# Kernel tuning notes

Measured on AMD Instinct MI355X. Metric: run time of the kernel, lower is better.

The kernel has to match this reference:

```python
import jax, jax.numpy as jnp
import numpy as np

B = 65536      # batch of (state, action) pairs
DIM_S = 64     # input feature dim
DIM_C = 8      # number of options / experts
H = 256        # hidden width (two hidden layers)


def setup_inputs() -> dict:
    key = jax.random.key(0)
    ks = jax.random.split(key, 7)
    s = 0.05  # small init scale
    st = jax.random.normal(ks[0], (B, DIM_S), dtype=jnp.float32)
    # Batched expert weights: one slice per expert (dim_c experts).
    W1 = jax.random.normal(ks[1], (DIM_C, DIM_S, H), dtype=jnp.float32) * s
    b1 = jax.random.normal(ks[2], (DIM_C, H), dtype=jnp.float32) * s
    W2 = jax.random.normal(ks[3], (DIM_C, H, H), dtype=jnp.float32) * s
    b2 = jax.random.normal(ks[4], (DIM_C, H), dtype=jnp.float32) * s
    W3 = jax.random.normal(ks[5], (DIM_C, H, 1), dtype=jnp.float32) * s
    b3 = jax.random.normal(ks[6], (DIM_C, 1), dtype=jnp.float32) * s
    return {"st": st, "W1": W1, "b1": b1, "W2": W2, "b2": b2,
            "W3": W3, "b3": b3}


def reference(st, W1, b1, W2, b2, W3, b3):
    # Equivalent of torch.stack([m(st) for m in self.discriminator], dim=1):
    # every expert MLP (dim_s -> H -> H -> 1, ReLU) applied to the same st,
    # expressed as batched GEMMs over the expert axis c.
    h = jax.nn.relu(jnp.einsum('bs,csh->bch', st, W1) + b1[None])   # [B, C, H]
    h = jax.nn.relu(jnp.einsum('bch,chk->bck', h, W2) + b2[None])   # [B, C, H]
    d = jnp.einsum('bch,cho->bco', h, W3) + b3[None]                # [B, C, 1]
    return d
```

## Files before the change

### kernel.cpp

```cpp
#include <hip/hip_runtime.h>
#include <hip/hip_bf16.h>

typedef __bf16 bf16x8 __attribute__((ext_vector_type(8)));
typedef float  f32x4  __attribute__((ext_vector_type(4)));

static constexpr int S  = 64;
static constexpr int C  = 8;
static constexpr int HD = 256;

__device__ __forceinline__ unsigned short f2bf(float f) {
  __hip_bfloat16 b = __float2bfloat16(f);
  unsigned short u;
  __builtin_memcpy(&u, &b, 2);
  return u;
}

__device__ __forceinline__ void gl2lds16(const void* g, void* l) {
  __builtin_amdgcn_global_load_lds(
      (const __attribute__((address_space(1))) unsigned int*)g,
      (__attribute__((address_space(3))) unsigned int*)l, 16, 0, 0);
}

__global__ __launch_bounds__(256) void prep_weights(
    const float* __restrict__ W1, const float* __restrict__ W2,
    unsigned short* __restrict__ W1T, unsigned short* __restrict__ W2T)
{
  __shared__ float tile[32][33];
  const int tid = threadIdx.x, cl = tid & 31, r0 = tid >> 5;
  const int b = blockIdx.x;
  if (b < 512) {
    const int c = b >> 6, t = b & 63, kt = t >> 3, nt = t & 7;
    const float* src = W2 + c * 65536;
    #pragma unroll
    for (int i = 0; i < 4; ++i) {
      int r = r0 + 8 * i;
      tile[r][cl] = src[(kt * 32 + r) * 256 + nt * 32 + cl];
    }
    __syncthreads();
    unsigned short* dst = W2T + c * 65536;
    #pragma unroll
    for (int i = 0; i < 4; ++i) {
      int r = r0 + 8 * i;
      dst[(nt * 32 + r) * 256 + kt * 32 + cl] = f2bf(tile[cl][r]);
    }
  } else {
    const int bb = b - 512;
    const int c = bb >> 4, t = bb & 15, st2 = t >> 3, ht = t & 7;
    const float* src = W1 + c * 16384;
    #pragma unroll
    for (int i = 0; i < 4; ++i) {
      int r = r0 + 8 * i;
      tile[r][cl] = src[(st2 * 32 + r) * 256 + ht * 32 + cl];
    }
    __syncthreads();
    unsigned short* dst = W1T + c * 16384;
    #pragma unroll
    for (int i = 0; i < 4; ++i) {
      int r = r0 + 8 * i;
      dst[(ht * 32 + r) * 64 + st2 * 32 + cl] = f2bf(tile[cl][r]);
    }
  }
}

__global__ __launch_bounds__(256, 2) void moe_fused(
    const float* __restrict__ st,
    const unsigned short* __restrict__ W1T,
    const unsigned short* __restrict__ W2T,
    const float* __restrict__ b1,
    const float* __restrict__ b2,
    const float* __restrict__ W3,
    const float* __restrict__ b3,
    float* __restrict__ out)
{
  constexpr int LDT = 72;

  __shared__ __align__(16) unsigned short sT[256 * LDT];
  __shared__ __align__(16) unsigned short sU[2 * 32 * 256];

  const int tid  = threadIdx.x;
  const int lane = tid & 63;
  const int wv   = tid >> 6;
  const int l15  = lane & 15;
  const int q    = lane >> 4;
  const int c    = blockIdx.x >> 8;
  const int row0 = (blockIdx.x & 255) * 256;

  const unsigned short* W1c = W1T + c * HD * S;
  const unsigned short* W2c = W2T + c * HD * HD;

  {
    #pragma unroll
    for (int it = 0; it < 8; ++it) {
      const int r = wv * 64 + it * 8 + (lane >> 3);
      const int g = lane & 7;
      const float4* p = reinterpret_cast<const float4*>(
          st + (size_t)(row0 + r) * S + g * 8);
      float4 x = p[0], y = p[1];
      union { uint4 u4; unsigned short us[8]; } pk;
      pk.us[0] = f2bf(x.x); pk.us[1] = f2bf(x.y); pk.us[2] = f2bf(x.z); pk.us[3] = f2bf(x.w);
      pk.us[4] = f2bf(y.x); pk.us[5] = f2bf(y.y); pk.us[6] = f2bf(y.z); pk.us[7] = f2bf(y.w);
      *reinterpret_cast<uint4*>(sU + r * 64 + ((g ^ (r & 7)) << 3)) = pk.u4;
    }
  }
  __asm__ __volatile__("s_waitcnt lgkmcnt(0)" ::: "memory");

  bf16x8 aF[4][4][2];
  #pragma unroll
  for (int cc = 0; cc < 4; ++cc) {
    f32x4 bias[4];
    #pragma unroll
    for (int mt = 0; mt < 4; ++mt)
      bias[mt] = *reinterpret_cast<const f32x4*>(
          b1 + c * HD + cc * 64 + mt * 16 + q * 4);

    f32x4 acc[4][4];
    #pragma unroll
    for (int mt = 0; mt < 4; ++mt)
      #pragma unroll
      for (int nt = 0; nt < 4; ++nt)
        acc[mt][nt] = (f32x4){0.f, 0.f, 0.f, 0.f};

    #pragma unroll
    for (int ks = 0; ks < 2; ++ks) {
      bf16x8 aW[4];
      #pragma unroll
      for (int mt = 0; mt < 4; ++mt)
        aW[mt] = *reinterpret_cast<const bf16x8*>(
            W1c + (cc * 64 + mt * 16 + l15) * S + ks * 32 + q * 8);
      bf16x8 bB[4];
      #pragma unroll
      for (int nt = 0; nt < 4; ++nt) {
        const int r = wv * 64 + nt * 16 + l15;
        const int g = ks * 4 + q;
        bB[nt] = *reinterpret_cast<const bf16x8*>(
            sU + r * 64 + ((g ^ (r & 7)) << 3));
      }
      #pragma unroll
      for (int mt = 0; mt < 4; ++mt)
        #pragma unroll
        for (int nt = 0; nt < 4; ++nt)
          acc[mt][nt] = __builtin_amdgcn_mfma_f32_16x16x32_bf16(
              aW[mt], bB[nt], acc[mt][nt], 0, 0, 0);
    }

    #pragma unroll
    for (int mt = 0; mt < 4; ++mt) {
      #pragma unroll
      for (int nt = 0; nt < 4; ++nt) {
        ushort4 pk;
        float v0 = acc[mt][nt][0] + bias[mt][0]; v0 = v0 > 0.f ? v0 : 0.f;
        float v1 = acc[mt][nt][1] + bias[mt][1]; v1 = v1 > 0.f ? v1 : 0.f;
        float v2 = acc[mt][nt][2] + bias[mt][2]; v2 = v2 > 0.f ? v2 : 0.f;
        float v3 = acc[mt][nt][3] + bias[mt][3]; v3 = v3 > 0.f ? v3 : 0.f;
        pk.x = f2bf(v0); pk.y = f2bf(v1); pk.z = f2bf(v2); pk.w = f2bf(v3);
        *reinterpret_cast<ushort4*>(
            sT + (wv * 64 + nt * 16 + l15) * LDT + mt * 16 + q * 4) = pk;
      }
    }
    __asm__ __volatile__("s_waitcnt lgkmcnt(0)" ::: "memory");
    #pragma unroll
    for (int rt = 0; rt < 4; ++rt)
      #pragma unroll
      for (int k2 = 0; k2 < 2; ++k2)
        aF[cc][rt][k2] = *reinterpret_cast<const bf16x8*>(
            sT + (wv * 64 + rt * 16 + l15) * LDT + k2 * 32 + q * 8);
    __asm__ __volatile__("s_waitcnt lgkmcnt(0)" ::: "memory");
  }

  float pb2v[8][2], pw3v[8][2];
  #pragma unroll
  for (int ch = 0; ch < 8; ++ch)
    #pragma unroll
    for (int ct = 0; ct < 2; ++ct) {
      const int n = ch * 32 + ct * 16 + l15;
      pb2v[ch][ct] = b2[c * HD + n];
      pw3v[ch][ct] = W3[c * HD + n];
    }
  const float bb3 = b3[c];

  __syncthreads();

  #pragma unroll
  for (int pc = 0; pc < 2; ++pc) {
    unsigned short* buf = sU + pc * (32 * 256);
    #pragma unroll
    for (int i = 0; i < 4; ++i) {
      const int b2i = wv * 4 + i;
      const int r   = b2i * 2 + (lane >> 5);
      const int j   = (lane & 31) ^ (r & 7);
      gl2lds16(W2c + (pc * 32 + r) * 256 + j * 8, buf + b2i * 512);
    }
  }
  __syncthreads();

  float dacc[4][4];
  #pragma unroll
  for (int rt = 0; rt < 4; ++rt)
    #pragma unroll
    for (int r = 0; r < 4; ++r) dacc[rt][r] = 0.f;

  #pragma unroll
  for (int ch = 0; ch < 8; ++ch) {
    const unsigned short* buf = sU + (ch & 1) * (32 * 256);

    f32x4 acc[4][2];
    #pragma unroll
    for (int rt = 0; rt < 4; ++rt)
      #pragma unroll
      for (int ct = 0; ct < 2; ++ct)
        acc[rt][ct] = (f32x4){0.f, 0.f, 0.f, 0.f};

    #pragma unroll
    for (int ks = 0; ks < 8; ++ks) {
      const int jj = ks * 4 + q;
      const int cc = ks >> 1, k2 = ks & 1;
      #pragma unroll
      for (int ct = 0; ct < 2; ++ct) {
        const int nl = ct * 16 + l15;
        bf16x8 b = *reinterpret_cast<const bf16x8*>(
            buf + nl * 256 + ((jj ^ (l15 & 7)) << 3));
        #pragma unroll
        for (int rt = 0; rt < 4; ++rt)
          acc[rt][ct] = __builtin_amdgcn_mfma_f32_16x16x32_bf16(
              aF[cc][rt][k2], b, acc[rt][ct], 0, 0, 0);
      }
    }

    #pragma unroll
    for (int ct = 0; ct < 2; ++ct) {
      const float bias = pb2v[ch][ct];
      const float w3v  = pw3v[ch][ct];
      #pragma unroll
      for (int rt = 0; rt < 4; ++rt)
        #pragma unroll
        for (int r = 0; r < 4; ++r) {
          float v = acc[rt][ct][r] + bias;
          v = v > 0.f ? v : 0.f;
          dacc[rt][r] += v * w3v;
        }
    }

    __syncthreads();
    if (ch < 6) {
      unsigned short* nbuf = sU + (ch & 1) * (32 * 256);
      #pragma unroll
      for (int i = 0; i < 4; ++i) {
        const int b2i = wv * 4 + i;
        const int r   = b2i * 2 + (lane >> 5);
        const int j   = (lane & 31) ^ (r & 7);
        gl2lds16(W2c + ((ch + 2) * 32 + r) * 256 + j * 8, nbuf + b2i * 512);
      }
    }
  }

  #pragma unroll
  for (int rt = 0; rt < 4; ++rt)
    #pragma unroll
    for (int r = 0; r < 4; ++r) {
      float v = dacc[rt][r];
      v += __shfl_xor(v, 1);
      v += __shfl_xor(v, 2);
      v += __shfl_xor(v, 4);
      v += __shfl_xor(v, 8);
      dacc[rt][r] = v;
    }

  if (l15 == 0) {
    const int rbase = row0 + wv * 64 + q * 4;
    #pragma unroll
    for (int rt = 0; rt < 4; ++rt)
      #pragma unroll
      for (int r = 0; r < 4; ++r)
        out[(rbase + rt * 16 + r) * C + c] = dacc[rt][r] + bb3;
  }
}

extern "C" void kernel_launch(void* const* d_in, const int* in_sizes, int n_in,
                              void* d_out, int out_size, void* d_ws, size_t ws_size,
                              hipStream_t stream)
{
  const float* st = (const float*)d_in[0];
  const float* W1 = (const float*)d_in[1];
  const float* b1 = (const float*)d_in[2];
  const float* W2 = (const float*)d_in[3];
  const float* b2 = (const float*)d_in[4];
  const float* W3 = (const float*)d_in[5];
  const float* b3 = (const float*)d_in[6];
  float* out = (float*)d_out;

  unsigned short* W1T = (unsigned short*)d_ws;
  unsigned short* W2T = W1T + C * HD * S;

  prep_weights<<<dim3(640), dim3(256), 0, stream>>>(W1, W2, W1T, W2T);
  moe_fused<<<dim3(2048), dim3(256), 0, stream>>>(st, W1T, W2T, b1, b2, W3, b3, out);
}
```

Measured before the change: 169.5 us.

## Halve rows per block, load inputs straight to registers, raise occupancy

Each block now handles 128 rows instead of 256, and the grid doubles. Block order is changed so the 8 experts sharing a row tile are adjacent, which improves L2 reuse of st. The st tile is converted and loaded directly into MFMA B-fragment registers instead of staging through LDS, and one barrier is removed. Smaller sT and fewer accumulators allow 3 blocks per CU, at the cost of loading each W2 chunk into LDS for half as many rows, which lowers weight reuse per block.

```diff
diff --git a/kernel.cpp b/kernel.cpp
--- a/kernel.cpp
+++ b/kernel.cpp
@@ -62,7 +62,7 @@
   }
 }
 
-__global__ __launch_bounds__(256, 2) void moe_fused(
+__global__ __launch_bounds__(256, 3) void moe_fused(
     const float* __restrict__ st,
     const unsigned short* __restrict__ W1T,
     const unsigned short* __restrict__ W2T,
@@ -74,7 +74,7 @@
 {
   constexpr int LDT = 72;
 
-  __shared__ __align__(16) unsigned short sT[256 * LDT];
+  __shared__ __align__(16) unsigned short sT[128 * LDT];
   __shared__ __align__(16) unsigned short sU[2 * 32 * 256];
 
   const int tid  = threadIdx.x;
@@ -82,29 +82,29 @@
   const int wv   = tid >> 6;
   const int l15  = lane & 15;
   const int q    = lane >> 4;
-  const int c    = blockIdx.x >> 8;
-  const int row0 = (blockIdx.x & 255) * 256;
+  const int c    = blockIdx.x & 7;
+  const int row0 = (blockIdx.x >> 3) * 128;
+  const int wrow = row0 + wv * 32;
 
   const unsigned short* W1c = W1T + c * HD * S;
   const unsigned short* W2c = W2T + c * HD * HD;
 
-  {
-    #pragma unroll
-    for (int it = 0; it < 8; ++it) {
-      const int r = wv * 64 + it * 8 + (lane >> 3);
-      const int g = lane & 7;
-      const float4* p = reinterpret_cast<const float4*>(
-          st + (size_t)(row0 + r) * S + g * 8);
+  bf16x8 bB[2][2];
+  #pragma unroll
+  for (int nt = 0; nt < 2; ++nt) {
+    const float* rp = st + (size_t)(wrow + nt * 16 + l15) * S;
+    #pragma unroll
+    for (int ks = 0; ks < 2; ++ks) {
+      const float4* p = reinterpret_cast<const float4*>(rp + ks * 32 + q * 8);
       float4 x = p[0], y = p[1];
-      union { uint4 u4; unsigned short us[8]; } pk;
+      union { bf16x8 v; unsigned short us[8]; } pk;
       pk.us[0] = f2bf(x.x); pk.us[1] = f2bf(x.y); pk.us[2] = f2bf(x.z); pk.us[3] = f2bf(x.w);
       pk.us[4] = f2bf(y.x); pk.us[5] = f2bf(y.y); pk.us[6] = f2bf(y.z); pk.us[7] = f2bf(y.w);
-      *reinterpret_cast<uint4*>(sU + r * 64 + ((g ^ (r & 7)) << 3)) = pk.u4;
-    }
-  }
-  __asm__ __volatile__("s_waitcnt lgkmcnt(0)" ::: "memory");
-
-  bf16x8 aF[4][4][2];
+      bB[ks][nt] = pk.v;
+    }
+  }
+
+  bf16x8 aF[4][2][2];
   #pragma unroll
   for (int cc = 0; cc < 4; ++cc) {
     f32x4 bias[4];
@@ -113,11 +113,11 @@
       bias[mt] = *reinterpret_cast<const f32x4*>(
           b1 + c * HD + cc * 64 + mt * 16 + q * 4);
 
-    f32x4 acc[4][4];
+    f32x4 acc[4][2];
     #pragma unroll
     for (int mt = 0; mt < 4; ++mt)
       #pragma unroll
-      for (int nt = 0; nt < 4; ++nt)
+      for (int nt = 0; nt < 2; ++nt)
         acc[mt][nt] = (f32x4){0.f, 0.f, 0.f, 0.f};
 
     #pragma unroll
@@ -127,26 +127,18 @@
       for (int mt = 0; mt < 4; ++mt)
         aW[mt] = *reinterpret_cast<const bf16x8*>(
             W1c + (cc * 64 + mt * 16 + l15) * S + ks * 32 + q * 8);
-      bf16x8 bB[4];
-      #pragma unroll
-      for (int nt = 0; nt < 4; ++nt) {
-        const int r = wv * 64 + nt * 16 + l15;
-        const int g = ks * 4 + q;
-        bB[nt] = *reinterpret_cast<const bf16x8*>(
-            sU + r * 64 + ((g ^ (r & 7)) << 3));
-      }
       #pragma unroll
       for (int mt = 0; mt < 4; ++mt)
         #pragma unroll
-        for (int nt = 0; nt < 4; ++nt)
+        for (int nt = 0; nt < 2; ++nt)
           acc[mt][nt] = __builtin_amdgcn_mfma_f32_16x16x32_bf16(
-              aW[mt], bB[nt], acc[mt][nt], 0, 0, 0);
+              aW[mt], bB[ks][nt], acc[mt][nt], 0, 0, 0);
     }
 
     #pragma unroll
     for (int mt = 0; mt < 4; ++mt) {
       #pragma unroll
-      for (int nt = 0; nt < 4; ++nt) {
+      for (int nt = 0; nt < 2; ++nt) {
         ushort4 pk;
         float v0 = acc[mt][nt][0] + bias[mt][0]; v0 = v0 > 0.f ? v0 : 0.f;
         float v1 = acc[mt][nt][1] + bias[mt][1]; v1 = v1 > 0.f ? v1 : 0.f;
@@ -154,16 +146,16 @@
         float v3 = acc[mt][nt][3] + bias[mt][3]; v3 = v3 > 0.f ? v3 : 0.f;
         pk.x = f2bf(v0); pk.y = f2bf(v1); pk.z = f2bf(v2); pk.w = f2bf(v3);
         *reinterpret_cast<ushort4*>(
-            sT + (wv * 64 + nt * 16 + l15) * LDT + mt * 16 + q * 4) = pk;
+            sT + (wv * 32 + nt * 16 + l15) * LDT + mt * 16 + q * 4) = pk;
       }
     }
     __asm__ __volatile__("s_waitcnt lgkmcnt(0)" ::: "memory");
     #pragma unroll
-    for (int rt = 0; rt < 4; ++rt)
+    for (int rt = 0; rt < 2; ++rt)
       #pragma unroll
       for (int k2 = 0; k2 < 2; ++k2)
         aF[cc][rt][k2] = *reinterpret_cast<const bf16x8*>(
-            sT + (wv * 64 + rt * 16 + l15) * LDT + k2 * 32 + q * 8);
+            sT + (wv * 32 + rt * 16 + l15) * LDT + k2 * 32 + q * 8);
     __asm__ __volatile__("s_waitcnt lgkmcnt(0)" ::: "memory");
   }
 
@@ -178,8 +170,6 @@
     }
   const float bb3 = b3[c];
 
-  __syncthreads();
-
   #pragma unroll
   for (int pc = 0; pc < 2; ++pc) {
     unsigned short* buf = sU + pc * (32 * 256);
@@ -193,9 +183,9 @@
   }
   __syncthreads();
 
-  float dacc[4][4];
-  #pragma unroll
-  for (int rt = 0; rt < 4; ++rt)
+  float dacc[2][4];
+  #pragma unroll
+  for (int rt = 0; rt < 2; ++rt)
     #pragma unroll
     for (int r = 0; r < 4; ++r) dacc[rt][r] = 0.f;
 
@@ -203,9 +193,9 @@
   for (int ch = 0; ch < 8; ++ch) {
     const unsigned short* buf = sU + (ch & 1) * (32 * 256);
 
-    f32x4 acc[4][2];
-    #pragma unroll
-    for (int rt = 0; rt < 4; ++rt)
+    f32x4 acc[2][2];
+    #pragma unroll
+    for (int rt = 0; rt < 2; ++rt)
       #pragma unroll
       for (int ct = 0; ct < 2; ++ct)
         acc[rt][ct] = (f32x4){0.f, 0.f, 0.f, 0.f};
@@ -220,7 +210,7 @@
         bf16x8 b = *reinterpret_cast<const bf16x8*>(
             buf + nl * 256 + ((jj ^ (l15 & 7)) << 3));
         #pragma unroll
-        for (int rt = 0; rt < 4; ++rt)
+        for (int rt = 0; rt < 2; ++rt)
           acc[rt][ct] = __builtin_amdgcn_mfma_f32_16x16x32_bf16(
               aF[cc][rt][k2], b, acc[rt][ct], 0, 0, 0);
       }
@@ -231,7 +221,7 @@
       const float bias = pb2v[ch][ct];
       const float w3v  = pw3v[ch][ct];
       #pragma unroll
-      for (int rt = 0; rt < 4; ++rt)
+      for (int rt = 0; rt < 2; ++rt)
         #pragma unroll
         for (int r = 0; r < 4; ++r) {
           float v = acc[rt][ct][r] + bias;
@@ -254,7 +244,7 @@
   }
 
   #pragma unroll
-  for (int rt = 0; rt < 4; ++rt)
+  for (int rt = 0; rt < 2; ++rt)
     #pragma unroll
     for (int r = 0; r < 4; ++r) {
       float v = dacc[rt][r];
@@ -266,12 +256,12 @@
     }
 
   if (l15 == 0) {
-    const int rbase = row0 + wv * 64 + q * 4;
-    #pragma unroll
-    for (int rt = 0; rt < 4; ++rt)
+    const int rbase = wrow + q * 4;
+    #pragma unroll
+    for (int rt = 0; rt < 2; ++rt)
       #pragma unroll
       for (int r = 0; r < 4; ++r)
-        out[(rbase + rt * 16 + r) * C + c] = dacc[rt][r] + bb3;
+        out[(size_t)(rbase + rt * 16 + r) * C + c] = dacc[rt][r] + bb3;
   }
 }
 
@@ -292,5 +282,5 @@
   unsigned short* W2T = W1T + C * HD * S;
 
   prep_weights<<<dim3(640), dim3(256), 0, stream>>>(W1, W2, W1T, W2T);
-  moe_fused<<<dim3(2048), dim3(256), 0, stream>>>(st, W1T, W2T, b1, b2, W3, b3, out);
-}
+  moe_fused<<<dim3(4096), dim3(256), 0, stream>>>(st, W1T, W2T, b1, b2, W3, b3, out);
+}
```

Result: slower. 207.4 us (+22.3%).
